# Optimization experiments

Measured on AMD Instinct MI355X. Metric: run time of the kernel, lower is better.

The kernel has to match this reference:

```python
import jax, jax.numpy as jnp
import numpy as np

N = 100000
E = 1600000
D_IN = 128
HID = 128
OUT = 64


def _sage_conv(x, edge_index, W_l, W_r, b, num_nodes):
    # PyG SAGEConv (aggr='mean'): out = lin_l(mean_{j in N(i)} x_j) + lin_r(x_i)
    src, dst = edge_index[0], edge_index[1]
    msgs = x[src]  # [E, d] gather from source nodes
    summed = jax.ops.segment_sum(msgs, dst, num_segments=num_nodes)  # [N, d]
    cnt = jax.ops.segment_sum(jnp.ones((msgs.shape[0],), x.dtype), dst, num_segments=num_nodes)
    agg = summed / jnp.maximum(cnt, 1.0)[:, None]  # mean; isolated nodes -> 0
    return agg @ W_l + b + x @ W_r


def setup_inputs() -> dict:
    key = jax.random.key(0)
    ks = jax.random.split(key, 8)
    x = jax.random.normal(ks[0], (N, D_IN), dtype=jnp.float32)
    edge_index = jax.random.randint(ks[1], (2, E), 0, N, dtype=jnp.int64)
    s1 = 1.0 / np.sqrt(D_IN)
    s2 = 1.0 / np.sqrt(HID)
    W_l1 = jax.random.uniform(ks[2], (D_IN, HID), jnp.float32, -s1, s1)
    W_r1 = jax.random.uniform(ks[3], (D_IN, HID), jnp.float32, -s1, s1)
    b1 = jnp.zeros((HID,), jnp.float32)
    W_l2 = jax.random.uniform(ks[4], (HID, OUT), jnp.float32, -s2, s2)
    W_r2 = jax.random.uniform(ks[5], (HID, OUT), jnp.float32, -s2, s2)
    b2 = jnp.zeros((OUT,), jnp.float32)
    return {"x": x, "edge_index": edge_index, "W_l1": W_l1, "W_r1": W_r1,
            "b1": b1, "W_l2": W_l2, "W_r2": W_r2, "b2": b2}


def reference(x, edge_index, W_l1, W_r1, b1, W_l2, W_r2, b2):
    h = _sage_conv(x, edge_index, W_l1, W_r1, b1, N)
    h = jax.nn.relu(h)
    out = _sage_conv(h, edge_index, W_l2, W_r2, b2, N)
    return out
```

## Files before the change

### kernel.cpp

```cpp
#include <hip/hip_runtime.h>
#include <hip/hip_fp16.h>

typedef __attribute__((ext_vector_type(8))) short bf16x8;
typedef __attribute__((ext_vector_type(4))) float f32x4;

__device__ __forceinline__ f32x4 mfma16(bf16x8 a, bf16x8 b, f32x4 c) {
    return __builtin_amdgcn_mfma_f32_16x16x32_bf16(a, b, c, 0, 0, 0);
}

__device__ __forceinline__ unsigned short bf16_rte(float f) {
    unsigned int u = __float_as_uint(f);
    unsigned int r = (u + 0x7FFFu + ((u >> 16) & 1u)) >> 16;
    return (unsigned short)r;
}
__device__ __forceinline__ float bf16_f(unsigned short h) {
    return __uint_as_float(((unsigned int)h) << 16);
}

__device__ __forceinline__ void split8h(bf16x8 raw, bf16x8& hi, bf16x8& lo) {
#pragma unroll
    for (int j = 0; j < 8; ++j) {
        float f = __half2float(__ushort_as_half((unsigned short)raw[j]));
        unsigned short h = bf16_rte(f);
        hi[j] = (short)h;
        lo[j] = (short)bf16_rte(f - bf16_f(h));
    }
}

__device__ __forceinline__ void acc8(uint4 r, float4& A0, float4& A1) {
    float2 v0 = __half22float2(*(const __half2*)&r.x);
    float2 v1 = __half22float2(*(const __half2*)&r.y);
    float2 v2 = __half22float2(*(const __half2*)&r.z);
    float2 v3 = __half22float2(*(const __half2*)&r.w);
    A0.x += v0.x; A0.y += v0.y; A0.z += v1.x; A0.w += v1.y;
    A1.x += v2.x; A1.y += v2.y; A1.z += v3.x; A1.w += v3.y;
}

__device__ __forceinline__ void acc4(uint2 r, float4& A) {
    float2 v0 = __half22float2(*(const __half2*)&r.x);
    float2 v1 = __half22float2(*(const __half2*)&r.y);
    A.x += v0.x; A.y += v0.y; A.z += v1.x; A.w += v1.y;
}

#define MAXNB 1024

__global__ __launch_bounds__(256) void k_prep(
    const float* __restrict__ Wl1, const float* __restrict__ Wr1,
    const float* __restrict__ Wl2, const float* __restrict__ Wr2,
    unsigned short* __restrict__ w1ah, unsigned short* __restrict__ w1al,
    unsigned short* __restrict__ w1bh, unsigned short* __restrict__ w1bl,
    unsigned short* __restrict__ w2ah, unsigned short* __restrict__ w2al,
    unsigned short* __restrict__ w2bh, unsigned short* __restrict__ w2bl,
    const float* __restrict__ x, unsigned short* __restrict__ x16,
    const int* __restrict__ dst, int* __restrict__ bcnt,
    int E, int chunk, int xb, int nb, int total8) {
    __shared__ int hh[MAXNB];
    int b = blockIdx.x;
    int t = threadIdx.x;
    if (b < 192) {
        const float* W;
        unsigned short *hi, *lo;
        int F, e;
        if (b < 64)       { W = Wl1; hi = w1ah; lo = w1al; F = 128; e = b * 256 + t; }
        else if (b < 128) { W = Wr1; hi = w1bh; lo = w1bl; F = 128; e = (b - 64) * 256 + t; }
        else if (b < 160) { W = Wl2; hi = w2ah; lo = w2al; F = 64;  e = (b - 128) * 256 + t; }
        else              { W = Wr2; hi = w2bh; lo = w2bl; F = 64;  e = (b - 160) * 256 + t; }
        if (e >= 128 * F) return;
        int col = e >> 7, k = e & 127;
        float v = W[(size_t)k * F + col];
        unsigned short h = bf16_rte(v);
        hi[e] = h;
        lo[e] = bf16_rte(v - bf16_f(h));
    } else if (b < 192 + xb) {
        int i = (b - 192) * 256 + t;
        if (i >= total8) return;
        const float4* xp = (const float4*)x + (size_t)i * 2;
        float4 a = xp[0], bb = xp[1];
        bf16x8 o;
        o[0] = (short)__half_as_ushort(__float2half_rn(a.x));
        o[1] = (short)__half_as_ushort(__float2half_rn(a.y));
        o[2] = (short)__half_as_ushort(__float2half_rn(a.z));
        o[3] = (short)__half_as_ushort(__float2half_rn(a.w));
        o[4] = (short)__half_as_ushort(__float2half_rn(bb.x));
        o[5] = (short)__half_as_ushort(__float2half_rn(bb.y));
        o[6] = (short)__half_as_ushort(__float2half_rn(bb.z));
        o[7] = (short)__half_as_ushort(__float2half_rn(bb.w));
        *(bf16x8*)&x16[(size_t)i * 8] = o;
    } else {
        int cb = b - 192 - xb;
        for (int i = t; i < nb; i += 256) hh[i] = 0;
        __syncthreads();
        int base = cb * chunk;
        int end = min(base + chunk, E);
        for (int i = base + t; i < end; i += 256) atomicAdd(&hh[dst[i] >> 7], 1);
        __syncthreads();
        for (int i = t; i < nb; i += 256)
            if (hh[i]) atomicAdd(&bcnt[i], hh[i]);
    }
}


__global__ void k_bscan(const int* __restrict__ bcnt, int* __restrict__ boff,
                        int* __restrict__ bcur, int nb) {
    __shared__ int sh[1024];
    int t = threadIdx.x;
    int v = (t < nb) ? bcnt[t] : 0;
    sh[t] = v;
    __syncthreads();
    for (int off = 1; off < 1024; off <<= 1) {
        int u = (t >= off) ? sh[t - off] : 0;
        __syncthreads();
        sh[t] += u;
        __syncthreads();
    }
    if (t < nb) {
        int ex = sh[t] - v;
        boff[t] = ex;
        bcur[t] = ex;
    }
}

__global__ __launch_bounds__(256) void k_bscatter(
    const int* __restrict__ src, const int* __restrict__ dst,
    int* __restrict__ bcur, int2* __restrict__ pairs, int E, int chunk, int nb) {
    __shared__ int h[MAXNB];
    __shared__ int curs[MAXNB];
    int t = threadIdx.x;
    for (int i = t; i < nb; i += 256) h[i] = 0;
    __syncthreads();
    int base = blockIdx.x * chunk;
    int end = min(base + chunk, E);
    for (int i = base + t; i < end; i += 256) atomicAdd(&h[dst[i] >> 7], 1);
    __syncthreads();
    for (int i = t; i < nb; i += 256)
        curs[i] = h[i] ? atomicAdd(&bcur[i], h[i]) : 0;
    __syncthreads();
    for (int i = base + t; i < end; i += 256) {
        int d = dst[i];
        int p = atomicAdd(&curs[d >> 7], 1);
        pairs[p] = make_int2(d, src[i]);
    }
}

__global__ __launch_bounds__(256) void k_build(
    const int2* __restrict__ pairs, const int* __restrict__ boff,
    int* __restrict__ csr, int* __restrict__ start, int* __restrict__ deg,
    int n, int nb, int E) {
    __shared__ int scnt[128];
    __shared__ int soff[128];
    __shared__ int cur[128];
    int b = blockIdx.x;
    int t = threadIdx.x;
    int base = boff[b];
    int end = (b + 1 < nb) ? boff[b + 1] : E;
    if (t < 128) scnt[t] = 0;
    __syncthreads();
    for (int i = base + t; i < end; i += 256) {
        int2 e = pairs[i];
        atomicAdd(&scnt[e.x & 127], 1);
    }
    __syncthreads();
    if (t < 128) soff[t] = scnt[t];
    __syncthreads();
    for (int off = 1; off < 128; off <<= 1) {
        int val = 0;
        if (t < 128 && t >= off) val = soff[t - off];
        __syncthreads();
        if (t < 128) soff[t] += val;
        __syncthreads();
    }
    if (t < 128) {
        int c = scnt[t];
        int ex = soff[t] - c;
        int node = b * 128 + t;
        if (node < n) {
            start[node] = base + ex;
            deg[node] = c;
        }
        cur[t] = base + ex;
    }
    __syncthreads();
    for (int i = base + t; i < end; i += 256) {
        int2 e = pairs[i];
        int p = atomicAdd(&cur[e.x & 127], 1);
        csr[p] = e.y;
    }
}

#define SR 40

__global__ __launch_bounds__(256) void aggF(
    const unsigned short* __restrict__ tab, const int* __restrict__ csr,
    const int* __restrict__ start, const int* __restrict__ deg,
    unsigned short* __restrict__ outm, int n) {
    int gid = blockIdx.x * blockDim.x + threadIdx.x;
    int wave = gid >> 6, lane = gid & 63;
    int sub = lane >> 4, fl = lane & 15;
    int node = wave * 4 + sub;
    if (node >= n) return;
    int s = start[node], d = deg[node];
    float4 A0 = {0.f, 0.f, 0.f, 0.f}, A1 = {0.f, 0.f, 0.f, 0.f};
    int j = 0;
    if (d >= 4) {
        int i0 = csr[s], i1 = csr[s + 1], i2 = csr[s + 2], i3 = csr[s + 3];
        for (; j + 8 <= d; j += 4) {
            int n0 = csr[s + j + 4], n1 = csr[s + j + 5];
            int n2 = csr[s + j + 6], n3 = csr[s + j + 7];
            uint4 r0 = ((const uint4*)(tab + (size_t)i0 * 128))[fl];
            uint4 r1 = ((const uint4*)(tab + (size_t)i1 * 128))[fl];
            uint4 r2 = ((const uint4*)(tab + (size_t)i2 * 128))[fl];
            uint4 r3 = ((const uint4*)(tab + (size_t)i3 * 128))[fl];
            acc8(r0, A0, A1); acc8(r1, A0, A1);
            acc8(r2, A0, A1); acc8(r3, A0, A1);
            i0 = n0; i1 = n1; i2 = n2; i3 = n3;
        }
        {
            uint4 r0 = ((const uint4*)(tab + (size_t)i0 * 128))[fl];
            uint4 r1 = ((const uint4*)(tab + (size_t)i1 * 128))[fl];
            uint4 r2 = ((const uint4*)(tab + (size_t)i2 * 128))[fl];
            uint4 r3 = ((const uint4*)(tab + (size_t)i3 * 128))[fl];
            acc8(r0, A0, A1); acc8(r1, A0, A1);
            acc8(r2, A0, A1); acc8(r3, A0, A1);
            j += 4;
        }
    }
    for (; j < d; ++j)
        acc8(((const uint4*)(tab + (size_t)csr[s + j] * 128))[fl], A0, A1);
    float inv = 1.0f / (float)max(d, 1);
    __half2 h0 = __floats2half2_rn(A0.x * inv, A0.y * inv);
    __half2 h1 = __floats2half2_rn(A0.z * inv, A0.w * inv);
    __half2 h2 = __floats2half2_rn(A1.x * inv, A1.y * inv);
    __half2 h3 = __floats2half2_rn(A1.z * inv, A1.w * inv);
    uint4 w;
    w.x = *(unsigned int*)&h0;
    w.y = *(unsigned int*)&h1;
    w.z = *(unsigned int*)&h2;
    w.w = *(unsigned int*)&h3;
    *(uint4*)&outm[(size_t)node * 128 + fl * 8] = w;
}

__global__ __launch_bounds__(256, 2) void fused12(
    const unsigned short* __restrict__ X, const unsigned short* __restrict__ XM,
    const unsigned short* __restrict__ W0H, const unsigned short* __restrict__ W0L,
    const unsigned short* __restrict__ W1H, const unsigned short* __restrict__ W1L,
    const float* __restrict__ b1,
    const unsigned short* __restrict__ W2aH, const unsigned short* __restrict__ W2aL,
    const unsigned short* __restrict__ W2bH, const unsigned short* __restrict__ W2bL,
    const float* __restrict__ b2,
    unsigned short* __restrict__ p16, float* __restrict__ outF, int n) {
    constexpr int CT = 2;
    __shared__ unsigned short aHi[4][64 * SR], aLo[4][64 * SR];

    int t = threadIdx.x;
    int wv = t >> 6, l = t & 63, q = l >> 4, nl = l & 15;
    int wc = wv * 32;
    int node0 = blockIdx.x * 64;
    int sn = t >> 2, q4 = t & 3;
    int gn = min(node0 + sn, n - 1);

    bf16x8 s1r[4];
    {
        const unsigned short* p = XM + (size_t)gn * 128 + q4 * 8;
#pragma unroll
        for (int c = 0; c < 4; ++c) s1r[c] = *(const bf16x8*)(p + c * 32);
    }
    bf16x8 w1h0[CT], w1l0[CT];
#pragma unroll
    for (int uu = 0; uu < CT; ++uu) {
        int base = (wc + uu * 16 + nl) * 128 + q * 8;
        w1h0[uu] = *(const bf16x8*)&W1H[base];
        w1l0[uu] = *(const bf16x8*)&W1L[base];
    }

    {
        const unsigned short* p = X + (size_t)gn * 128 + q4 * 8;
        bf16x8 r[4];
#pragma unroll
        for (int c = 0; c < 4; ++c) r[c] = *(const bf16x8*)(p + c * 32);
        int base = sn * SR + q4 * 8;
#pragma unroll
        for (int c = 0; c < 4; ++c) {
            bf16x8 hi, lo;
            split8h(r[c], hi, lo);
            *(bf16x8*)&aHi[c][base] = hi;
            *(bf16x8*)&aLo[c][base] = lo;
        }
    }

    f32x4 acc[4][CT];
#pragma unroll
    for (int a = 0; a < 4; ++a)
#pragma unroll
        for (int b = 0; b < CT; ++b) acc[a][b] = (f32x4){0.f, 0.f, 0.f, 0.f};

    bf16x8 wh[2][CT], wl[2][CT];
#pragma unroll
    for (int uu = 0; uu < CT; ++uu) {
        int base = (wc + uu * 16 + nl) * 128 + q * 8;
        wh[0][uu] = *(const bf16x8*)&W0H[base];
        wl[0][uu] = *(const bf16x8*)&W0L[base];
    }
    __syncthreads();

#pragma unroll
    for (int c = 0; c < 4; ++c) {
        if (c < 3) {
#pragma unroll
            for (int uu = 0; uu < CT; ++uu) {
                int base = (wc + uu * 16 + nl) * 128 + (c + 1) * 32 + q * 8;
                wh[(c + 1) & 1][uu] = *(const bf16x8*)&W0H[base];
                wl[(c + 1) & 1][uu] = *(const bf16x8*)&W0L[base];
            }
        }
        bf16x8 ah[4], al[4];
#pragma unroll
        for (int tt = 0; tt < 4; ++tt) {
            int off = (tt * 16 + nl) * SR + q * 8;
            ah[tt] = *(const bf16x8*)&aHi[c][off];
            al[tt] = *(const bf16x8*)&aLo[c][off];
        }
        int cb = c & 1;
#pragma unroll
        for (int tt = 0; tt < 4; ++tt)
#pragma unroll
            for (int uu = 0; uu < CT; ++uu) {
                f32x4 a = acc[tt][uu];
                a = mfma16(al[tt], wh[cb][uu], a);
                a = mfma16(ah[tt], wl[cb][uu], a);
                a = mfma16(ah[tt], wh[cb][uu], a);
                acc[tt][uu] = a;
            }
    }
    __syncthreads();

    {
        int base = sn * SR + q4 * 8;
#pragma unroll
        for (int c = 0; c < 4; ++c) {
            bf16x8 hi, lo;
            split8h(s1r[c], hi, lo);
            *(bf16x8*)&aHi[c][base] = hi;
            *(bf16x8*)&aLo[c][base] = lo;
        }
    }
#pragma unroll
    for (int uu = 0; uu < CT; ++uu) { wh[0][uu] = w1h0[uu]; wl[0][uu] = w1l0[uu]; }
    __syncthreads();

#pragma unroll
    for (int c = 0; c < 4; ++c) {
        if (c < 3) {
#pragma unroll
            for (int uu = 0; uu < CT; ++uu) {
                int base = (wc + uu * 16 + nl) * 128 + (c + 1) * 32 + q * 8;
                wh[(c + 1) & 1][uu] = *(const bf16x8*)&W1H[base];
                wl[(c + 1) & 1][uu] = *(const bf16x8*)&W1L[base];
            }
        }
        bf16x8 ah[4], al[4];
#pragma unroll
        for (int tt = 0; tt < 4; ++tt) {
            int off = (tt * 16 + nl) * SR + q * 8;
            ah[tt] = *(const bf16x8*)&aHi[c][off];
            al[tt] = *(const bf16x8*)&aLo[c][off];
        }
        int cb = c & 1;
#pragma unroll
        for (int tt = 0; tt < 4; ++tt)
#pragma unroll
            for (int uu = 0; uu < CT; ++uu) {
                f32x4 a = acc[tt][uu];
                a = mfma16(al[tt], wh[cb][uu], a);
                a = mfma16(ah[tt], wl[cb][uu], a);
                a = mfma16(ah[tt], wh[cb][uu], a);
                acc[tt][uu] = a;
            }
    }
    __syncthreads();

    unsigned short* tb = &aHi[0][0];
#pragma unroll
    for (int uu = 0; uu < CT; ++uu) {
        int col = wc + uu * 16 + nl;
        float bv = b1[col];
#pragma unroll
        for (int tt = 0; tt < 4; ++tt)
#pragma unroll
            for (int r = 0; r < 4; ++r) {
                float vv = fmaxf(acc[tt][uu][r] + bv, 0.f);
                tb[(tt * 16 + q * 4 + r) * 136 + col] =
                    __half_as_ushort(__float2half_rn(vv));
            }
    }
    __syncthreads();

    bf16x8 hreg[4];
    {
        const unsigned short* sp = tb + sn * 136 + q4 * 8;
#pragma unroll
        for (int c = 0; c < 4; ++c) hreg[c] = *(const bf16x8*)(sp + c * 32);
    }
    __syncthreads();

    {
        int base = sn * SR + q4 * 8;
#pragma unroll
        for (int c = 0; c < 4; ++c) {
            bf16x8 hi, lo;
            split8h(hreg[c], hi, lo);
            *(bf16x8*)&aHi[c][base] = hi;
            *(bf16x8*)&aLo[c][base] = lo;
        }
    }
    int ysel = wv >> 1;
    int wc2 = (wv & 1) * 32;
    const unsigned short* W2H = ysel ? W2bH : W2aH;
    const unsigned short* W2L = ysel ? W2bL : W2aL;
#pragma unroll
    for (int uu = 0; uu < CT; ++uu) {
        int base = (wc2 + uu * 16 + nl) * 128 + q * 8;
        wh[0][uu] = *(const bf16x8*)&W2H[base];
        wl[0][uu] = *(const bf16x8*)&W2L[base];
    }
#pragma unroll
    for (int a = 0; a < 4; ++a)
#pragma unroll
        for (int b = 0; b < CT; ++b) acc[a][b] = (f32x4){0.f, 0.f, 0.f, 0.f};
    __syncthreads();

#pragma unroll
    for (int c = 0; c < 4; ++c) {
        if (c < 3) {
#pragma unroll
            for (int uu = 0; uu < CT; ++uu) {
                int base = (wc2 + uu * 16 + nl) * 128 + (c + 1) * 32 + q * 8;
                wh[(c + 1) & 1][uu] = *(const bf16x8*)&W2H[base];
                wl[(c + 1) & 1][uu] = *(const bf16x8*)&W2L[base];
            }
        }
        bf16x8 ah[4], al[4];
#pragma unroll
        for (int tt = 0; tt < 4; ++tt) {
            int off = (tt * 16 + nl) * SR + q * 8;
            ah[tt] = *(const bf16x8*)&aHi[c][off];
            al[tt] = *(const bf16x8*)&aLo[c][off];
        }
        int cb = c & 1;
#pragma unroll
        for (int tt = 0; tt < 4; ++tt)
#pragma unroll
            for (int uu = 0; uu < CT; ++uu) {
                f32x4 a = acc[tt][uu];
                a = mfma16(al[tt], wh[cb][uu], a);
                a = mfma16(ah[tt], wl[cb][uu], a);
                a = mfma16(ah[tt], wh[cb][uu], a);
                acc[tt][uu] = a;
            }
    }
    __syncthreads();

    unsigned short* tbu = &aHi[0][0];
    float* tbf = (float*)&aLo[0][0];
#pragma unroll
    for (int uu = 0; uu < CT; ++uu) {
        int col = wc2 + uu * 16 + nl;
        if (ysel) {
            float bv = b2[col];
#pragma unroll
            for (int tt = 0; tt < 4; ++tt)
#pragma unroll
                for (int r = 0; r < 4; ++r)
                    tbf[(tt * 16 + q * 4 + r) * 68 + col] = acc[tt][uu][r] + bv;
        } else {
#pragma unroll
            for (int tt = 0; tt < 4; ++tt)
#pragma unroll
                for (int r = 0; r < 4; ++r)
                    tbu[(tt * 16 + q * 4 + r) * 72 + col] =
                        __half_as_ushort(__float2half_rn(acc[tt][uu][r]));
        }
    }
    __syncthreads();
    int node = node0 + sn;
    if (node < n) {
        const unsigned short* spu = tbu + sn * 72 + q4 * 16;
        unsigned short* dpu = p16 + (size_t)node * 64 + q4 * 16;
        *(bf16x8*)dpu = *(const bf16x8*)spu;
        *(bf16x8*)(dpu + 8) = *(const bf16x8*)(spu + 8);
        const float* spf = tbf + sn * 68 + q4 * 16;
        float* dpf = outF + (size_t)node * 64 + q4 * 16;
#pragma unroll
        for (int i = 0; i < 4; ++i) *(float4*)(dpf + i * 4) = *(const float4*)(spf + i * 4);
    }
}

__global__ __launch_bounds__(256) void aggP(
    const unsigned short* __restrict__ tab, const int* __restrict__ csr,
    const int* __restrict__ start, const int* __restrict__ deg,
    float* __restrict__ outF, int n) {
    int gid = blockIdx.x * blockDim.x + threadIdx.x;
    int wave = gid >> 6, lane = gid & 63;
    int sub = lane >> 4, fl = lane & 15;
    int node = wave * 4 + sub;
    if (node >= n) return;
    int s = start[node], d = deg[node];
    float4 A = {0.f, 0.f, 0.f, 0.f};
    int j = 0;
    if (d >= 8) {
        int idx[8];
#pragma unroll
        for (int k = 0; k < 8; ++k) idx[k] = csr[s + k];
        for (; j + 16 <= d; j += 8) {
            uint2 rr[8];
#pragma unroll
            for (int k = 0; k < 8; ++k)
                rr[k] = ((const uint2*)(tab + (size_t)idx[k] * 64))[fl];
#pragma unroll
            for (int k = 0; k < 8; ++k) idx[k] = csr[s + j + 8 + k];
#pragma unroll
            for (int k = 0; k < 8; ++k) acc4(rr[k], A);
        }
        {
            uint2 rr[8];
#pragma unroll
            for (int k = 0; k < 8; ++k)
                rr[k] = ((const uint2*)(tab + (size_t)idx[k] * 64))[fl];
#pragma unroll
            for (int k = 0; k < 8; ++k) acc4(rr[k], A);
            j += 8;
        }
    }
    for (; j < d; ++j)
        acc4(((const uint2*)(tab + (size_t)csr[s + j] * 64))[fl], A);
    float inv = 1.0f / (float)max(d, 1);
    float* op = outF + (size_t)node * 64 + fl * 4;
    float4 cur = *(float4*)op;
    cur.x += A.x * inv;
    cur.y += A.y * inv;
    cur.z += A.z * inv;
    cur.w += A.w * inv;
    *(float4*)op = cur;
}


extern "C" void kernel_launch(void* const* d_in, const int* in_sizes, int n_in,
                              void* d_out, int out_size, void* d_ws, size_t ws_size,
                              hipStream_t stream) {
    const float* x   = (const float*)d_in[0];
    const int*   ei  = (const int*)d_in[1];
    const float* Wl1 = (const float*)d_in[2];
    const float* Wr1 = (const float*)d_in[3];
    const float* b1  = (const float*)d_in[4];
    const float* Wl2 = (const float*)d_in[5];
    const float* Wr2 = (const float*)d_in[6];
    const float* b2  = (const float*)d_in[7];
    float* out = (float*)d_out;

    int Nn = in_sizes[0] / 128;
    int E  = in_sizes[1] / 2;
    const int* src = ei;
    const int* dst = ei + E;
    int nb = (Nn + 127) / 128;

    char* ws = (char*)d_ws;
    auto alloc = [&](size_t bytes) -> char* {
        char* pp = ws;
        ws += (bytes + 255) / 256 * 256;
        return pp;
    };
    int* bcnt   = (int*)alloc((size_t)nb * 4);
    int* boff   = (int*)alloc((size_t)nb * 4);
    int* bcur   = (int*)alloc((size_t)nb * 4);
    int* start  = (int*)alloc((size_t)Nn * 4);
    int* deg    = (int*)alloc((size_t)Nn * 4);
    int* csr    = (int*)alloc((size_t)E * 4);
    unsigned short* x16  = (unsigned short*)alloc((size_t)Nn * 128 * 2);
    unsigned short* xm16 = (unsigned short*)alloc((size_t)Nn * 128 * 2);
    unsigned short* p16  = (unsigned short*)alloc((size_t)Nn * 64 * 2);
    unsigned short* w1ah = (unsigned short*)alloc(128 * 128 * 2);
    unsigned short* w1al = (unsigned short*)alloc(128 * 128 * 2);
    unsigned short* w1bh = (unsigned short*)alloc(128 * 128 * 2);
    unsigned short* w1bl = (unsigned short*)alloc(128 * 128 * 2);
    unsigned short* w2ah = (unsigned short*)alloc(64 * 128 * 2);
    unsigned short* w2al = (unsigned short*)alloc(64 * 128 * 2);
    unsigned short* w2bh = (unsigned short*)alloc(64 * 128 * 2);
    unsigned short* w2bl = (unsigned short*)alloc(64 * 128 * 2);
    int2* pairs = (int2*)p16;

    hipMemsetAsync(bcnt, 0, (size_t)nb * 4, stream);

    int total8 = Nn * 16;
    int xb = (total8 + 255) / 256;
    int chunk = (E + 255) / 256;
    k_prep<<<192 + xb + 256, 256, 0, stream>>>(
        Wl1, Wr1, Wl2, Wr2,
        w1ah, w1al, w1bh, w1bl, w2ah, w2al, w2bh, w2bl,
        x, x16, dst, bcnt, E, chunk, xb, nb, total8);

    k_bscan<<<1, 1024, 0, stream>>>(bcnt, boff, bcur, nb);
    k_bscatter<<<256, 256, 0, stream>>>(src, dst, bcur, pairs, E, chunk, nb);
    k_build<<<nb, 256, 0, stream>>>(pairs, boff, csr, start, deg, Nn, nb, E);

    int gb = (Nn + 63) / 64;
    int ga = (Nn + 15) / 16;
    aggF<<<ga, 256, 0, stream>>>(x16, csr, start, deg, xm16, Nn);
    fused12<<<gb, 256, 0, stream>>>(x16, xm16,
                                    w1bh, w1bl, w1ah, w1al, b1,
                                    w2ah, w2al, w2bh, w2bl, b2,
                                    p16, out, Nn);
    aggP<<<ga, 256, 0, stream>>>(p16, csr, start, deg, out, Nn);
}
```

Before: 328.1 us.

## Shrink fused GEMM LDS to two-chunk ping-pong and raise occupancy

The fused two-layer GEMM kernel now stages only two K-chunks of hi/lo activations in LDS at a time. Staging of the next chunk overlaps the MFMA work on the current one, which roughly halves shared memory and lets launch bounds ask for four blocks per CU instead of two. The fp32 output is now written directly from the accumulators rather than through LDS. Separately, the edge bucketing kernels use 1024 chunks instead of 256 for more parallelism. This adds more barriers per phase, and the direct output stores are less coalesced.

```diff
diff --git a/kernel.cpp b/kernel.cpp
--- a/kernel.cpp
+++ b/kernel.cpp
@@ -239,7 +239,7 @@
     *(uint4*)&outm[(size_t)node * 128 + fl * 8] = w;
 }
 
-__global__ __launch_bounds__(256, 2) void fused12(
+__global__ __launch_bounds__(256, 4) void fused12(
     const unsigned short* __restrict__ X, const unsigned short* __restrict__ XM,
     const unsigned short* __restrict__ W0H, const unsigned short* __restrict__ W0L,
     const unsigned short* __restrict__ W1H, const unsigned short* __restrict__ W1L,
@@ -249,42 +249,27 @@
     const float* __restrict__ b2,
     unsigned short* __restrict__ p16, float* __restrict__ outF, int n) {
     constexpr int CT = 2;
-    __shared__ unsigned short aHi[4][64 * SR], aLo[4][64 * SR];
+    __shared__ unsigned short lds[4 * 64 * SR];
+    unsigned short* hi0 = lds;
+    unsigned short* hi1 = lds + 64 * SR;
+    unsigned short* lo0 = lds + 2 * 64 * SR;
+    unsigned short* lo1 = lds + 3 * 64 * SR;
 
     int t = threadIdx.x;
     int wv = t >> 6, l = t & 63, q = l >> 4, nl = l & 15;
-    int wc = wv * 32;
     int node0 = blockIdx.x * 64;
     int sn = t >> 2, q4 = t & 3;
     int gn = min(node0 + sn, n - 1);
-
-    bf16x8 s1r[4];
-    {
-        const unsigned short* p = XM + (size_t)gn * 128 + q4 * 8;
-#pragma unroll
-        for (int c = 0; c < 4; ++c) s1r[c] = *(const bf16x8*)(p + c * 32);
-    }
-    bf16x8 w1h0[CT], w1l0[CT];
-#pragma unroll
-    for (int uu = 0; uu < CT; ++uu) {
-        int base = (wc + uu * 16 + nl) * 128 + q * 8;
-        w1h0[uu] = *(const bf16x8*)&W1H[base];
-        w1l0[uu] = *(const bf16x8*)&W1L[base];
-    }
-
+    int sbase = sn * SR + q4 * 8;
+
+    bf16x8 xr[4], s1r[4];
     {
         const unsigned short* p = X + (size_t)gn * 128 + q4 * 8;
-        bf16x8 r[4];
-#pragma unroll
-        for (int c = 0; c < 4; ++c) r[c] = *(const bf16x8*)(p + c * 32);
-        int base = sn * SR + q4 * 8;
-#pragma unroll
-        for (int c = 0; c < 4; ++c) {
-            bf16x8 hi, lo;
-            split8h(r[c], hi, lo);
-            *(bf16x8*)&aHi[c][base] = hi;
-            *(bf16x8*)&aLo[c][base] = lo;
-        }
+#pragma unroll
+        for (int c = 0; c < 4; ++c) xr[c] = *(const bf16x8*)(p + c * 32);
+        const unsigned short* pm = XM + (size_t)gn * 128 + q4 * 8;
+#pragma unroll
+        for (int c = 0; c < 4; ++c) s1r[c] = *(const bf16x8*)(pm + c * 32);
     }
 
     f32x4 acc[4][CT];
@@ -293,95 +278,70 @@
 #pragma unroll
         for (int b = 0; b < CT; ++b) acc[a][b] = (f32x4){0.f, 0.f, 0.f, 0.f};
 
-    bf16x8 wh[2][CT], wl[2][CT];
+    bf16x8 whA[CT], wlA[CT], whB[CT], wlB[CT];
+    int wcX = wv * 32;
+
+#define LOAD_W(AH, AL, WHp, WLp, CC)                                       \
+    {                                                                      \
+        _Pragma("unroll") for (int uu = 0; uu < CT; ++uu) {                \
+            int wb = (wcX + uu * 16 + nl) * 128 + (CC) * 32 + q * 8;       \
+            AH[uu] = *(const bf16x8*)&(WHp)[wb];                           \
+            AL[uu] = *(const bf16x8*)&(WLp)[wb];                           \
+        }                                                                  \
+    }
+
+#define STAGE_CHUNK(HP, LP, RAW)                                           \
+    {                                                                      \
+        bf16x8 _hi, _lo;                                                   \
+        split8h(RAW, _hi, _lo);                                            \
+        *(bf16x8*)&(HP)[sbase] = _hi;                                      \
+        *(bf16x8*)&(LP)[sbase] = _lo;                                      \
+    }
+
+#define MFMA_CHUNK(HP, LP, WHR, WLR)                                       \
+    {                                                                      \
+        bf16x8 ah[4], al[4];                                               \
+        _Pragma("unroll") for (int tt = 0; tt < 4; ++tt) {                 \
+            int off = (tt * 16 + nl) * SR + q * 8;                         \
+            ah[tt] = *(const bf16x8*)&(HP)[off];                           \
+            al[tt] = *(const bf16x8*)&(LP)[off];                           \
+        }                                                                  \
+        _Pragma("unroll") for (int tt = 0; tt < 4; ++tt)                   \
+            _Pragma("unroll") for (int uu = 0; uu < CT; ++uu) {            \
+                f32x4 a = acc[tt][uu];                                     \
+                a = mfma16(al[tt], WHR[uu], a);                            \
+                a = mfma16(ah[tt], WLR[uu], a);                            \
+                a = mfma16(ah[tt], WHR[uu], a);                            \
+                acc[tt][uu] = a;                                           \
+            }                                                              \
+    }
+
+#define PHASE(RSRC, WHp, WLp)                                              \
+    LOAD_W(whA, wlA, WHp, WLp, 0);                                         \
+    STAGE_CHUNK(hi0, lo0, RSRC[0]);                                        \
+    __syncthreads();                                                       \
+    LOAD_W(whB, wlB, WHp, WLp, 1);                                         \
+    STAGE_CHUNK(hi1, lo1, RSRC[1]);                                        \
+    MFMA_CHUNK(hi0, lo0, whA, wlA);                                        \
+    __syncthreads();                                                       \
+    LOAD_W(whA, wlA, WHp, WLp, 2);                                         \
+    STAGE_CHUNK(hi0, lo0, RSRC[2]);                                        \
+    MFMA_CHUNK(hi1, lo1, whB, wlB);                                        \
+    __syncthreads();                                                       \
+    LOAD_W(whB, wlB, WHp, WLp, 3);                                         \
+    STAGE_CHUNK(hi1, lo1, RSRC[3]);                                        \
+    MFMA_CHUNK(hi0, lo0, whA, wlA);                                        \
+    __syncthreads();                                                       \
+    MFMA_CHUNK(hi1, lo1, whB, wlB);                                        \
+    __syncthreads();
+
+    PHASE(xr, W0H, W0L);
+    PHASE(s1r, W1H, W1L);
+
+    unsigned short* tb = lds;
 #pragma unroll
     for (int uu = 0; uu < CT; ++uu) {
-        int base = (wc + uu * 16 + nl) * 128 + q * 8;
-        wh[0][uu] = *(const bf16x8*)&W0H[base];
-        wl[0][uu] = *(const bf16x8*)&W0L[base];
-    }
-    __syncthreads();
-
-#pragma unroll
-    for (int c = 0; c < 4; ++c) {
-        if (c < 3) {
-#pragma unroll
-            for (int uu = 0; uu < CT; ++uu) {
-                int base = (wc + uu * 16 + nl) * 128 + (c + 1) * 32 + q * 8;
-                wh[(c + 1) & 1][uu] = *(const bf16x8*)&W0H[base];
-                wl[(c + 1) & 1][uu] = *(const bf16x8*)&W0L[base];
-            }
-        }
-        bf16x8 ah[4], al[4];
-#pragma unroll
-        for (int tt = 0; tt < 4; ++tt) {
-            int off = (tt * 16 + nl) * SR + q * 8;
-            ah[tt] = *(const bf16x8*)&aHi[c][off];
-            al[tt] = *(const bf16x8*)&aLo[c][off];
-        }
-        int cb = c & 1;
-#pragma unroll
-        for (int tt = 0; tt < 4; ++tt)
-#pragma unroll
-            for (int uu = 0; uu < CT; ++uu) {
-                f32x4 a = acc[tt][uu];
-                a = mfma16(al[tt], wh[cb][uu], a);
-                a = mfma16(ah[tt], wl[cb][uu], a);
-                a = mfma16(ah[tt], wh[cb][uu], a);
-                acc[tt][uu] = a;
-            }
-    }
-    __syncthreads();
-
-    {
-        int base = sn * SR + q4 * 8;
-#pragma unroll
-        for (int c = 0; c < 4; ++c) {
-            bf16x8 hi, lo;
-            split8h(s1r[c], hi, lo);
-            *(bf16x8*)&aHi[c][base] = hi;
-            *(bf16x8*)&aLo[c][base] = lo;
-        }
-    }
-#pragma unroll
-    for (int uu = 0; uu < CT; ++uu) { wh[0][uu] = w1h0[uu]; wl[0][uu] = w1l0[uu]; }
-    __syncthreads();
-
-#pragma unroll
-    for (int c = 0; c < 4; ++c) {
-        if (c < 3) {
-#pragma unroll
-            for (int uu = 0; uu < CT; ++uu) {
-                int base = (wc + uu * 16 + nl) * 128 + (c + 1) * 32 + q * 8;
-                wh[(c + 1) & 1][uu] = *(const bf16x8*)&W1H[base];
-                wl[(c + 1) & 1][uu] = *(const bf16x8*)&W1L[base];
-            }
-        }
-        bf16x8 ah[4], al[4];
-#pragma unroll
-        for (int tt = 0; tt < 4; ++tt) {
-            int off = (tt * 16 + nl) * SR + q * 8;
-            ah[tt] = *(const bf16x8*)&aHi[c][off];
-            al[tt] = *(const bf16x8*)&aLo[c][off];
-        }
-        int cb = c & 1;
-#pragma unroll
-        for (int tt = 0; tt < 4; ++tt)
-#pragma unroll
-            for (int uu = 0; uu < CT; ++uu) {
-                f32x4 a = acc[tt][uu];
-                a = mfma16(al[tt], wh[cb][uu], a);
-                a = mfma16(ah[tt], wl[cb][uu], a);
-                a = mfma16(ah[tt], wh[cb][uu], a);
-                acc[tt][uu] = a;
-            }
-    }
-    __syncthreads();
-
-    unsigned short* tb = &aHi[0][0];
-#pragma unroll
-    for (int uu = 0; uu < CT; ++uu) {
-        int col = wc + uu * 16 + nl;
+        int col = wcX + uu * 16 + nl;
         float bv = b1[col];
 #pragma unroll
         for (int tt = 0; tt < 4; ++tt)
@@ -393,7 +353,6 @@
             }
     }
     __syncthreads();
-
     bf16x8 hreg[4];
     {
         const unsigned short* sp = tb + sn * 136 + q4 * 8;
@@ -402,76 +361,39 @@
     }
     __syncthreads();
 
-    {
-        int base = sn * SR + q4 * 8;
-#pragma unroll
-        for (int c = 0; c < 4; ++c) {
-            bf16x8 hi, lo;
-            split8h(hreg[c], hi, lo);
-            *(bf16x8*)&aHi[c][base] = hi;
-            *(bf16x8*)&aLo[c][base] = lo;
-        }
-    }
+#pragma unroll
+    for (int a = 0; a < 4; ++a)
+#pragma unroll
+        for (int b = 0; b < CT; ++b) acc[a][b] = (f32x4){0.f, 0.f, 0.f, 0.f};
     int ysel = wv >> 1;
-    int wc2 = (wv & 1) * 32;
+    wcX = (wv & 1) * 32;
     const unsigned short* W2H = ysel ? W2bH : W2aH;
     const unsigned short* W2L = ysel ? W2bL : W2aL;
-#pragma unroll
-    for (int uu = 0; uu < CT; ++uu) {
-        int base = (wc2 + uu * 16 + nl) * 128 + q * 8;
-        wh[0][uu] = *(const bf16x8*)&W2H[base];
-        wl[0][uu] = *(const bf16x8*)&W2L[base];
-    }
-#pragma unroll
-    for (int a = 0; a < 4; ++a)
-#pragma unroll
-        for (int b = 0; b < CT; ++b) acc[a][b] = (f32x4){0.f, 0.f, 0.f, 0.f};
-    __syncthreads();
-
-#pragma unroll
-    for (int c = 0; c < 4; ++c) {
-        if (c < 3) {
-#pragma unroll
-            for (int uu = 0; uu < CT; ++uu) {
-                int base = (wc2 + uu * 16 + nl) * 128 + (c + 1) * 32 + q * 8;
-                wh[(c + 1) & 1][uu] = *(const bf16x8*)&W2H[base];
-                wl[(c + 1) & 1][uu] = *(const bf16x8*)&W2L[base];
-            }
-        }
-        bf16x8 ah[4], al[4];
-#pragma unroll
-        for (int tt = 0; tt < 4; ++tt) {
-            int off = (tt * 16 + nl) * SR + q * 8;
-            ah[tt] = *(const bf16x8*)&aHi[c][off];
-            al[tt] = *(const bf16x8*)&aLo[c][off];
-        }
-        int cb = c & 1;
-#pragma unroll
-        for (int tt = 0; tt < 4; ++tt)
-#pragma unroll
-            for (int uu = 0; uu < CT; ++uu) {
-                f32x4 a = acc[tt][uu];
-                a = mfma16(al[tt], wh[cb][uu], a);
-                a = mfma16(ah[tt], wl[cb][uu], a);
-                a = mfma16(ah[tt], wh[cb][uu], a);
-                acc[tt][uu] = a;
-            }
-    }
-    __syncthreads();
-
-    unsigned short* tbu = &aHi[0][0];
-    float* tbf = (float*)&aLo[0][0];
-#pragma unroll
-    for (int uu = 0; uu < CT; ++uu) {
-        int col = wc2 + uu * 16 + nl;
-        if (ysel) {
+    PHASE(hreg, W2H, W2L);
+
+#undef PHASE
+#undef MFMA_CHUNK
+#undef STAGE_CHUNK
+#undef LOAD_W
+
+    if (ysel) {
+#pragma unroll
+        for (int uu = 0; uu < CT; ++uu) {
+            int col = wcX + uu * 16 + nl;
             float bv = b2[col];
 #pragma unroll
             for (int tt = 0; tt < 4; ++tt)
 #pragma unroll
-                for (int r = 0; r < 4; ++r)
-                    tbf[(tt * 16 + q * 4 + r) * 68 + col] = acc[tt][uu][r] + bv;
-        } else {
+                for (int r = 0; r < 4; ++r) {
+                    int node = node0 + tt * 16 + q * 4 + r;
+                    if (node < n) outF[(size_t)node * 64 + col] = acc[tt][uu][r] + bv;
+                }
+        }
+    } else {
+        unsigned short* tbu = lds;
+#pragma unroll
+        for (int uu = 0; uu < CT; ++uu) {
+            int col = wcX + uu * 16 + nl;
 #pragma unroll
             for (int tt = 0; tt < 4; ++tt)
 #pragma unroll
@@ -481,16 +403,14 @@
         }
     }
     __syncthreads();
-    int node = node0 + sn;
-    if (node < n) {
-        const unsigned short* spu = tbu + sn * 72 + q4 * 16;
-        unsigned short* dpu = p16 + (size_t)node * 64 + q4 * 16;
-        *(bf16x8*)dpu = *(const bf16x8*)spu;
-        *(bf16x8*)(dpu + 8) = *(const bf16x8*)(spu + 8);
-        const float* spf = tbf + sn * 68 + q4 * 16;
-        float* dpf = outF + (size_t)node * 64 + q4 * 16;
-#pragma unroll
-        for (int i = 0; i < 4; ++i) *(float4*)(dpf + i * 4) = *(const float4*)(spf + i * 4);
+    {
+        int node = node0 + sn;
+        if (node < n) {
+            const unsigned short* spu = lds + sn * 72 + q4 * 16;
+            unsigned short* dpu = p16 + (size_t)node * 64 + q4 * 16;
+            *(bf16x8*)dpu = *(const bf16x8*)spu;
+            *(bf16x8*)(dpu + 8) = *(const bf16x8*)(spu + 8);
+        }
     }
 }
 
@@ -591,14 +511,15 @@
 
     int total8 = Nn * 16;
     int xb = (total8 + 255) / 256;
-    int chunk = (E + 255) / 256;
-    k_prep<<<192 + xb + 256, 256, 0, stream>>>(
+    int nchunks = 1024;
+    int chunk = (E + nchunks - 1) / nchunks;
+    k_prep<<<192 + xb + nchunks, 256, 0, stream>>>(
         Wl1, Wr1, Wl2, Wr2,
         w1ah, w1al, w1bh, w1bl, w2ah, w2al, w2bh, w2bl,
         x, x16, dst, bcnt, E, chunk, xb, nb, total8);
 
     k_bscan<<<1, 1024, 0, stream>>>(bcnt, boff, bcur, nb);
-    k_bscatter<<<256, 256, 0, stream>>>(src, dst, bcur, pairs, E, chunk, nb);
+    k_bscatter<<<nchunks, 256, 0, stream>>>(src, dst, bcur, pairs, E, chunk, nb);
     k_build<<<nb, 256, 0, stream>>>(pairs, boff, csr, start, deg, Nn, nb, E);
 
     int gb = (Nn + 63) / 64;
```

New measurement: 346.6 us. +5.6%, slower.
